# Performance work log

Hardware: AMD Instinct MI355X
Metric: run time of the kernel (lower is better)

The kernel has to match this reference:

```python
import math
import jax, jax.numpy as jnp
import numpy as np

NUM_HEADS = 32

def _alibi_slopes(n: int) -> jnp.ndarray:
    cp2 = 2 ** int(math.floor(math.log2(n)))
    base = 2.0 ** (-(2.0 ** (-(math.log2(cp2) - 3))))
    slopes = base ** np.arange(1, cp2 + 1, dtype=np.float64)
    if cp2 != n:
        extra_base = 2.0 ** (-(2.0 ** (-(math.log2(2 * cp2) - 3))))
        rem = min(cp2, n - cp2)
        slopes = np.concatenate([slopes, extra_base ** np.arange(1, 1 + 2 * rem, 2, dtype=np.float64)])
    return jnp.asarray(slopes, dtype=jnp.float32)


def setup_inputs() -> dict:
    key = jax.random.key(0)
    k1, k2, k3 = jax.random.split(key, 3)
    B, S, E, H, D = 2, 2048, 4096, NUM_HEADS, 128
    hidden_states = jax.random.normal(k1, (B, S, E), dtype=jnp.float32)
    # torch Linear y = x @ W^T; we store transposed weights [in, out]
    w_qkv = jax.random.normal(k2, (E, H * D + 2 * D), dtype=jnp.float32) * 0.02
    w_c = jax.random.normal(k3, (E, E), dtype=jnp.float32) * 0.02
    return {"hidden_states": hidden_states, "w_qkv": w_qkv, "w_c": w_c}


def reference(hidden_states, w_qkv, w_c):
    B, S, E = hidden_states.shape
    H = NUM_HEADS
    D = E // H
    scaling = D ** -0.5

    qkv = hidden_states @ w_qkv                      # [B,S,H*D+2D]
    q = qkv[..., : H * D].reshape(B, S, H, D)        # [B,S,H,D]
    k = qkv[..., H * D: H * D + D]                   # [B,S,D] single KV head (MQA)
    v = qkv[..., H * D + D:]                         # [B,S,D]

    pos = jnp.arange(S)
    slopes = _alibi_slopes(H)                        # [H]
    # ALiBi: slope * (k_pos - q_pos), <= 0 in the causal region
    bias = slopes[:, None, None] * (pos[None, None, :] - pos[None, :, None]).astype(jnp.float32)  # [H,S,S]

    scores = jnp.einsum('bqhd,bkd->bhqk', q, k) * scaling + bias[None]  # [B,H,S,S]
    causal = pos[:, None] >= pos[None, :]            # [S,S]
    scores = jnp.where(causal[None, None], scores, jnp.finfo(scores.dtype).min)
    probs = jax.nn.softmax(scores, axis=-1)
    attn = jnp.einsum('bhqk,bkd->bqhd', probs, v).reshape(B, S, E)
    return attn @ w_c
```

## Files before the change

kernel.cpp:

```cpp
#include <hip/hip_runtime.h>
#include <hip/hip_bf16.h>

typedef unsigned short u16;
typedef unsigned int u32;
typedef __attribute__((ext_vector_type(8))) short s16x8;
typedef __attribute__((ext_vector_type(4))) float f32x4;

#define MFMA_BF16(a, b, c) __builtin_amdgcn_mfma_f32_16x16x32_bf16(a, b, c, 0, 0, 0)

__device__ __forceinline__ u16 f2bf(float f) {
  union { float f; u32 u; } c; c.f = f;
  return (u16)((c.u + 0x7FFFu + ((c.u >> 16) & 1u)) >> 16);
}

__device__ __forceinline__ u32 pkbf(float a, float b) {
  float2 t; t.x = a; t.y = b;
  __hip_bfloat162 h = __float22bfloat162_rn(t);
  union { __hip_bfloat162 h; u32 u; } c; c.h = h; return c.u;
}

__device__ __forceinline__ void gll16(const void* g, void* l) {
  __builtin_amdgcn_global_load_lds((const __attribute__((address_space(1))) void*)g,
                                   (__attribute__((address_space(3))) void*)l, 16, 0, 0);
}

__device__ __forceinline__ f32x4 f4zero() { f32x4 z = {0.f, 0.f, 0.f, 0.f}; return z; }

__global__ void cvt_bf16_kernel(const float4* __restrict__ in, u16* __restrict__ out, int n4) {
  int i = blockIdx.x * 256 + threadIdx.x;
  if (i >= n4) return;
  float4 v = in[i];
  uint2 w;
  w.x = (u32)f2bf(v.x) | ((u32)f2bf(v.y) << 16);
  w.y = (u32)f2bf(v.z) | ((u32)f2bf(v.w) << 16);
  *reinterpret_cast<uint2*>(out + (size_t)i * 4) = w;
}

__global__ void transpose_cvt_kernel(const float* __restrict__ in, u16* __restrict__ out,
                                     int R, int C) {
  __shared__ float tile[32][33];
  int tx = threadIdx.x, ty = threadIdx.y;
  int r0 = blockIdx.y * 32, c0 = blockIdx.x * 32;
#pragma unroll
  for (int i = 0; i < 32; i += 8)
    tile[ty + i][tx] = in[(size_t)(r0 + ty + i) * C + c0 + tx];
  __syncthreads();
#pragma unroll
  for (int i = 0; i < 32; i += 8)
    out[(size_t)(c0 + ty + i) * R + r0 + tx] = f2bf(tile[tx][ty + i]);
}


#define BARRIER __builtin_amdgcn_s_barrier()
#define SCHEDB __builtin_amdgcn_sched_barrier(0)
#define PRIO1 __builtin_amdgcn_s_setprio(1)
#define PRIO0 __builtin_amdgcn_s_setprio(0)
#define VM6 asm volatile("s_waitcnt vmcnt(6)" ::: "memory")
#define VM0 asm volatile("s_waitcnt vmcnt(0)" ::: "memory")
#define NOPW do {} while (0)

#define PAB(P) ((P) * 8192)
#define PBB(P) (24576 + (P) * 16384)

#define RDAB(P) do { _Pragma("unroll")                                                   \
  for (int mi2 = 0; mi2 < 4; ++mi2)                                                      \
    a[mi2] = *(const s16x8*)(smem + PAB(P) + aOff + mi2*1024);                           \
  _Pragma("unroll")                                                                      \
  for (int ni2 = 0; ni2 < 8; ++ni2)                                                      \
    b[ni2] = *(const s16x8*)(smem + PBB(P) + bOff + ni2*1024);                           \
} while (0)

#define MFMA32 do { _Pragma("unroll")                                                    \
  for (int mi2 = 0; mi2 < 4; ++mi2) { _Pragma("unroll")                                  \
    for (int ni2 = 0; ni2 < 8; ++ni2)                                                    \
      acc[mi2][ni2] = MFMA_BF16(a[mi2], b[ni2], acc[mi2][ni2]);                          \
  } } while (0)

#define STAGE6(P, kn) do {                                                               \
  gll16(srcA + (kn), smem + PAB(P) + tt*16);                                             \
  gll16(srcA + (size_t)64 * K + (kn), smem + PAB(P) + 4096 + tt*16);                     \
  _Pragma("unroll")                                                                      \
  for (int j = 0; j < 4; ++j)                                                            \
    gll16(srcB0 + (size_t)(j * 64) * K + (kn), smem + PBB(P) + j*4096 + tt*16);          \
} while (0)

#define TILE_S(PR, PS, T) do {                                                           \
  s16x8 a[4], b[8];                                                                      \
  RDAB(PR);                                                                              \
  STAGE6(PS, ((T) + 2) * 32);                                                            \
  SCHEDB;                                                                                \
  PRIO1; MFMA32; PRIO0;                                                                  \
  SCHEDB;                                                                                \
  VM6;                                                                                   \
  BARRIER;                                                                               \
} while (0)

#define TILE_T(PR, WAIT) do {                                                            \
  s16x8 a[4], b[8];                                                                      \
  RDAB(PR);                                                                              \
  SCHEDB;                                                                                \
  PRIO1; MFMA32; PRIO0;                                                                  \
  SCHEDB;                                                                                \
  WAIT;                                                                                  \
  BARRIER;                                                                               \
} while (0)

template<int EPI>
__global__ __launch_bounds__(256, 2)
void gemm128_kernel(const u16* __restrict__ A, const u16* __restrict__ Bt,
                    float* __restrict__ Cf, u16* __restrict__ Cq,
                    u16* __restrict__ Ck, u16* __restrict__ Cvt,
                    int N, int K) {
  __shared__ __align__(16) char smem[73728];
  const int tt = threadIdx.x;
  const int w = tt >> 6, l = tt & 63;
  const int li = l & 15, g = l >> 4;
  const int wm = w >> 1, wn = w & 1;

  const int gx = gridDim.x;
  const int raw = blockIdx.y * gx + blockIdx.x;
  const int bn = raw >> 5;
  const int bm = ((raw >> 3) & 3) * 8 + (raw & 7);

  f32x4 acc[4][8];
#pragma unroll
  for (int i = 0; i < 4; ++i)
#pragma unroll
    for (int j = 0; j < 8; ++j) acc[i][j] = f4zero();

  const int sg = (tt & 7) ^ ((tt >> 3) & 7);
  const int ar = 2 * (tt >> 3) + (sg >> 2);
  const int aq = sg & 3;
  const u16* srcA = A + (size_t)(bm * 128 + ar) * K + aq * 8;
  const u16* srcB0 = Bt + (size_t)(bn * 256 + ar) * K + aq * 8;

  const int slot = (((li & 1) * 4 + g) ^ ((li >> 1) & 7)) * 16;
  const int aOff = wm * 4096 + (li >> 1) * 128 + slot;
  const int bOff = wn * 8192 + (li >> 1) * 128 + slot;

  STAGE6(0, 0);
  STAGE6(1, 32);
  VM6;
  BARRIER;

  for (int t3 = 0; t3 < 126; t3 += 3) {
    TILE_S(0, 2, t3);
    TILE_S(1, 0, t3 + 1);
    TILE_S(2, 1, t3 + 2);
  }
  TILE_T(0, VM0);
  TILE_T(1, NOPW);

#pragma unroll
  for (int mi = 0; mi < 4; ++mi) {
#pragma unroll
    for (int ni = 0; ni < 8; ++ni) {
      const int row0 = bm * 128 + wm * 64 + mi * 16 + g * 4;
      const int col = bn * 256 + wn * 128 + ni * 16 + li;
#pragma unroll
      for (int r = 0; r < 4; ++r) {
        const int m = row0 + r;
        const float v = acc[mi][ni][r];
        if (EPI == 0) {
          Cf[(size_t)m * N + col] = v;
        } else {
          const int bb2 = m >> 11, s = m & 2047;
          const int kt = s >> 5;
          const size_t tb = (size_t)(bb2 * 64 + kt);
          if (col < 4096) {
            Cq[(size_t)m * 4096 + col] = f2bf(v);
          } else if (col < 4224) {
            const int d = col - 4096, kr = s & 31;
            const int mk = kr >> 4, lii = kr & 15;
            const int kk = d >> 5, gg = (d >> 3) & 3, e = d & 7;
            Ck[(tb * 8 + mk * 4 + kk) * 512 + (gg * 16 + lii) * 8 + e] = f2bf(v);
          } else {
            const int d = col - 4224, kp = s & 31;
            const int mf = d >> 4, lii = d & 15;
            const int gg = kp >> 3, e = kp & 7;
            Cvt[(tb * 8 + mf) * 512 + (gg * 16 + lii) * 8 + e] = f2bf(v);
          }
        }
      }
    }
  }
}


__device__ __forceinline__ void load_ktile(s16x8 (&dst)[8], const u16* kf, size_t tb, int l) {
#pragma unroll
  for (int f = 0; f < 8; ++f)
    dst[f] = *(const s16x8*)&kf[(tb * 8 + f) * 512 + l * 8];
}

template<bool DIAG>
__device__ __forceinline__ void attn_tile(
    int kt, const u16* kf, const u16* vf, size_t bb64, int l, int li, int g,
    s16x8 (&use)[8], s16x8 (&fill)[8], bool do_fill,
    const s16x8 (&bq)[2][4], f32x4 (&acc)[8][2],
    float (&m_)[2], float (&lp)[2], float (&bias)[2],
    float c1, const float (&cjr)[8], float bstep, u16 (*Pw)[40]) {
  const size_t tb = bb64 + kt;
  s16x8 vr[8];
#pragma unroll
  for (int f = 0; f < 8; ++f)
    vr[f] = *(const s16x8*)&vf[(tb * 8 + f) * 512 + l * 8];
  if (do_fill) load_ktile(fill, kf, tb - 1, l);

  f32x4 sc[2][2];
  sc[0][0] = f4zero(); sc[0][1] = f4zero(); sc[1][0] = f4zero(); sc[1][1] = f4zero();
#pragma unroll
  for (int kk = 0; kk < 4; ++kk)
#pragma unroll
    for (int mk = 0; mk < 2; ++mk) {
      sc[mk][0] = MFMA_BF16(use[mk * 4 + kk], bq[0][kk], sc[mk][0]);
      sc[mk][1] = MFMA_BF16(use[mk * 4 + kk], bq[1][kk], sc[mk][1]);
    }

#pragma unroll
  for (int nq = 0; nq < 2; ++nq) {
    float sv[8];
    float pm = -3e38f;
    if (DIAG) {
#pragma unroll
      for (int mk = 0; mk < 2; ++mk)
#pragma unroll
        for (int r = 0; r < 4; ++r) {
          const int kd = mk * 16 + g * 4 + r - (nq * 16 + li);
          float s = fmaf(sc[mk][nq][r], c1, bias[nq] + cjr[mk * 4 + r]);
          s = (kd <= 0) ? s : -1e30f;
          sv[mk * 4 + r] = s;
          pm = fmaxf(pm, s);
        }
      pm = fmaxf(pm, __shfl_xor(pm, 16));
      pm = fmaxf(pm, __shfl_xor(pm, 32));
      m_[nq] = pm;
    } else {
#pragma unroll
      for (int mk = 0; mk < 2; ++mk)
#pragma unroll
        for (int r = 0; r < 4; ++r) {
          float s = fmaf(sc[mk][nq][r], c1, bias[nq] + cjr[mk * 4 + r]);
          sv[mk * 4 + r] = s;
          pm = fmaxf(pm, s);
        }
      if (__any(pm > m_[nq])) {
        pm = fmaxf(pm, __shfl_xor(pm, 16));
        pm = fmaxf(pm, __shfl_xor(pm, 32));
        const float nm = fmaxf(m_[nq], pm);
        const float scale = exp2f(m_[nq] - nm);
#pragma unroll
        for (int mf = 0; mf < 8; ++mf) acc[mf][nq] *= scale;
        lp[nq] *= scale;
        m_[nq] = nm;
      }
    }
    const float mref = m_[nq];
    float e[8];
#pragma unroll
    for (int j = 0; j < 8; ++j) e[j] = exp2f(sv[j] - mref);
    lp[nq] += ((e[0] + e[1]) + (e[2] + e[3])) + ((e[4] + e[5]) + (e[6] + e[7]));
#pragma unroll
    for (int mk = 0; mk < 2; ++mk) {
      uint2 wv;
      wv.x = pkbf(e[mk * 4 + 0], e[mk * 4 + 1]);
      wv.y = pkbf(e[mk * 4 + 2], e[mk * 4 + 3]);
      *reinterpret_cast<uint2*>(&Pw[nq * 16 + li][mk * 16 + g * 4]) = wv;
    }
    bias[nq] -= bstep;
  }

  s16x8 pb0 = *(const s16x8*)&Pw[li][g * 8];
  s16x8 pb1 = *(const s16x8*)&Pw[16 + li][g * 8];
#pragma unroll
  for (int mf = 0; mf < 8; ++mf) {
    acc[mf][0] = MFMA_BF16(vr[mf], pb0, acc[mf][0]);
    acc[mf][1] = MFMA_BF16(vr[mf], pb1, acc[mf][1]);
  }
}

__device__ __forceinline__ void attn_qtile(
    int qt, int h, int b, const u16* qbuf, const u16* kf, const u16* vf,
    u16* obuf, int l, int li, int g, float c1, float sl2, u16 (*Pw)[40]) {
  const int S = 2048;
  const int q0 = qt * 32;
  const size_t bb64 = (size_t)b * 64;

  s16x8 bq[2][4];
#pragma unroll
  for (int nq = 0; nq < 2; ++nq)
#pragma unroll
    for (int kk = 0; kk < 4; ++kk)
      bq[nq][kk] = *(const s16x8*)&qbuf[(size_t)(b * S + q0 + nq * 16 + li) * 4096
                                        + h * 128 + kk * 32 + g * 8];

  f32x4 acc[8][2];
#pragma unroll
  for (int mf = 0; mf < 8; ++mf) { acc[mf][0] = f4zero(); acc[mf][1] = f4zero(); }
  float m_[2] = {-3e38f, -3e38f};
  float lp[2] = {0.f, 0.f};

  float cjr[8];
#pragma unroll
  for (int j = 0; j < 8; ++j) cjr[j] = sl2 * (float)((j >> 2) * 16 + (j & 3));
  float bias[2];
#pragma unroll
  for (int nq = 0; nq < 2; ++nq)
    bias[nq] = sl2 * (float)(g * 4 - nq * 16 - li);
  const float bstep = sl2 * 32.f;

  s16x8 kA[8], kB[8];
  load_ktile(kA, kf, bb64 + qt, l);
  attn_tile<true>(qt, kf, vf, bb64, l, li, g, kA, kB, qt >= 1,
                  bq, acc, m_, lp, bias, c1, cjr, bstep, Pw);
  int kt = qt - 1;
  while (kt >= 1) {
    attn_tile<false>(kt, kf, vf, bb64, l, li, g, kB, kA, true,
                     bq, acc, m_, lp, bias, c1, cjr, bstep, Pw);
    attn_tile<false>(kt - 1, kf, vf, bb64, l, li, g, kA, kB, kt >= 2,
                     bq, acc, m_, lp, bias, c1, cjr, bstep, Pw);
    kt -= 2;
  }
  if (kt == 0)
    attn_tile<false>(0, kf, vf, bb64, l, li, g, kB, kA, false,
                     bq, acc, m_, lp, bias, c1, cjr, bstep, Pw);

#pragma unroll
  for (int nq = 0; nq < 2; ++nq) {
    float ls = lp[nq];
    ls += __shfl_xor(ls, 16);
    ls += __shfl_xor(ls, 32);
    const float inv = 1.f / ls;
    const size_t rowbase = (size_t)(b * S + q0 + nq * 16 + li) * 4096 + h * 128;
#pragma unroll
    for (int mf = 0; mf < 8; ++mf) {
      f32x4 v = acc[mf][nq];
      uint2 wv;
      wv.x = pkbf(v[0] * inv, v[1] * inv);
      wv.y = pkbf(v[2] * inv, v[3] * inv);
      *reinterpret_cast<uint2*>(&obuf[rowbase + mf * 16 + g * 4]) = wv;
    }
  }
}

__global__ __launch_bounds__(64, 2)
void attn_kernel(const u16* __restrict__ qbuf, const u16* __restrict__ kf,
                 const u16* __restrict__ vf, u16* __restrict__ obuf) {
  const int p = blockIdx.x, h = blockIdx.y, b = blockIdx.z;
  const int l = threadIdx.x, li = l & 15, g = l >> 4;
  const float L2E = 1.4426950408889634f;
  const float slope = exp2f(-0.25f * (float)(h + 1));
  const float c1 = 0.08838834764831845f * L2E;
  const float sl2 = slope * L2E;
  __shared__ __align__(16) u16 P[32][40];
  attn_qtile(63 - p, h, b, qbuf, kf, vf, obuf, l, li, g, c1, sl2, P);
  attn_qtile(p, h, b, qbuf, kf, vf, obuf, l, li, g, c1, sl2, P);
}

extern "C" void kernel_launch(void* const* d_in, const int* in_sizes, int n_in,
                              void* d_out, int out_size, void* d_ws, size_t ws_size,
                              hipStream_t stream) {
  (void)in_sizes; (void)n_in; (void)out_size; (void)ws_size;
  const float* hidden = (const float*)d_in[0];
  const float* w_qkv = (const float*)d_in[1];
  const float* w_c = (const float*)d_in[2];
  float* out = (float*)d_out;
  char* ws = (char*)d_ws;

  u16* hid_bf = (u16*)(ws + 0);
  u16* wT     = (u16*)(ws + 33554432);
  u16* qbuf   = (u16*)(ws + 69206016);
  u16* kbuf   = (u16*)(ws + 102760448);
  u16* vtbuf  = (u16*)(ws + 103809024);

  cvt_bf16_kernel<<<16384, 256, 0, stream>>>((const float4*)hidden, hid_bf, 4194304);
  transpose_cvt_kernel<<<dim3(136, 128), dim3(32, 8), 0, stream>>>(w_qkv, wT, 4096, 4352);
  gemm128_kernel<1><<<dim3(17, 32), 256, 0, stream>>>(hid_bf, wT, nullptr, qbuf, kbuf, vtbuf,
                                                      4352, 4096);
  attn_kernel<<<dim3(32, 32, 2), 64, 0, stream>>>(qbuf, kbuf, vtbuf, hid_bf);
  transpose_cvt_kernel<<<dim3(128, 128), dim3(32, 8), 0, stream>>>(w_c, wT, 4096, 4096);
  gemm128_kernel<0><<<dim3(16, 32), 256, 0, stream>>>(hid_bf, wT, out, nullptr, nullptr, nullptr,
                                                      4096, 4096);
}
```

Baseline: 479.9 us.

## Fuse fp32-to-bf16 hidden-state conversion into the QKV GEMM A-tile loads

Removes the separate conversion kernel that turned the fp32 hidden states into a bf16 workspace copy. The QKV GEMM now reads fp32 A rows into registers, converts them to bf16 in flight, and writes them to LDS after the MFMA block; B tiles still use direct global-to-LDS loads. This drops one full read and write pass over the activations and one kernel launch. In exchange, each of the 17 column blocks re-reads A in fp32, which doubles A traffic, and the extra live registers could hurt latency hiding at two blocks per SM.

```diff
diff --git a/kernel.cpp b/kernel.cpp
--- a/kernel.cpp
+++ b/kernel.cpp
@@ -25,16 +25,6 @@
 }
 
 __device__ __forceinline__ f32x4 f4zero() { f32x4 z = {0.f, 0.f, 0.f, 0.f}; return z; }
-
-__global__ void cvt_bf16_kernel(const float4* __restrict__ in, u16* __restrict__ out, int n4) {
-  int i = blockIdx.x * 256 + threadIdx.x;
-  if (i >= n4) return;
-  float4 v = in[i];
-  uint2 w;
-  w.x = (u32)f2bf(v.x) | ((u32)f2bf(v.y) << 16);
-  w.y = (u32)f2bf(v.z) | ((u32)f2bf(v.w) << 16);
-  *reinterpret_cast<uint2*>(out + (size_t)i * 4) = w;
-}
 
 __global__ void transpose_cvt_kernel(const float* __restrict__ in, u16* __restrict__ out,
                                      int R, int C) {
@@ -56,6 +46,7 @@
 #define PRIO1 __builtin_amdgcn_s_setprio(1)
 #define PRIO0 __builtin_amdgcn_s_setprio(0)
 #define VM6 asm volatile("s_waitcnt vmcnt(6)" ::: "memory")
+#define VM4 asm volatile("s_waitcnt vmcnt(4)" ::: "memory")
 #define VM0 asm volatile("s_waitcnt vmcnt(0)" ::: "memory")
 #define NOPW do {} while (0)
 
@@ -76,22 +67,45 @@
       acc[mi2][ni2] = MFMA_BF16(a[mi2], b[ni2], acc[mi2][ni2]);                          \
   } } while (0)
 
+#define STAGE_B4(P, kn) do { _Pragma("unroll")                                           \
+  for (int j = 0; j < 4; ++j)                                                            \
+    gll16(srcB0 + (size_t)(j * 64) * K + (kn), smem + PBB(P) + j*4096 + tt*16);          \
+} while (0)
+
 #define STAGE6(P, kn) do {                                                               \
   gll16(srcA + (kn), smem + PAB(P) + tt*16);                                             \
   gll16(srcA + (size_t)64 * K + (kn), smem + PAB(P) + 4096 + tt*16);                     \
-  _Pragma("unroll")                                                                      \
-  for (int j = 0; j < 4; ++j)                                                            \
-    gll16(srcB0 + (size_t)(j * 64) * K + (kn), smem + PBB(P) + j*4096 + tt*16);          \
+  STAGE_B4(P, kn);                                                                       \
+} while (0)
+
+#define A_LOADF(T) do {                                                                  \
+  f0a = *(const float4*)(srcAf0 + (size_t)(T) * 32);                                     \
+  f0b = *(const float4*)(srcAf0 + (size_t)(T) * 32 + 4);                                 \
+  f1a = *(const float4*)(srcAf1 + (size_t)(T) * 32);                                     \
+  f1b = *(const float4*)(srcAf1 + (size_t)(T) * 32 + 4);                                 \
+} while (0)
+
+#define A_WRITEF(P) do {                                                                 \
+  uint4 w0, w1;                                                                          \
+  w0.x = pkbf(f0a.x, f0a.y); w0.y = pkbf(f0a.z, f0a.w);                                  \
+  w0.z = pkbf(f0b.x, f0b.y); w0.w = pkbf(f0b.z, f0b.w);                                  \
+  w1.x = pkbf(f1a.x, f1a.y); w1.y = pkbf(f1a.z, f1a.w);                                  \
+  w1.z = pkbf(f1b.x, f1b.y); w1.w = pkbf(f1b.z, f1b.w);                                  \
+  *reinterpret_cast<uint4*>(smem + PAB(P) + tt*16) = w0;                                 \
+  *reinterpret_cast<uint4*>(smem + PAB(P) + 4096 + tt*16) = w1;                          \
 } while (0)
 
 #define TILE_S(PR, PS, T) do {                                                           \
   s16x8 a[4], b[8];                                                                      \
+  float4 f0a, f0b, f1a, f1b;                                                             \
+  if constexpr (EPI == 1) { A_LOADF((T) + 2); }                                          \
   RDAB(PR);                                                                              \
-  STAGE6(PS, ((T) + 2) * 32);                                                            \
+  if constexpr (EPI == 1) { STAGE_B4(PS, ((T) + 2) * 32); }                              \
+  else { STAGE6(PS, ((T) + 2) * 32); }                                                   \
   SCHEDB;                                                                                \
   PRIO1; MFMA32; PRIO0;                                                                  \
   SCHEDB;                                                                                \
-  VM6;                                                                                   \
+  if constexpr (EPI == 1) { A_WRITEF(PS); } else { VM6; }                                \
   BARRIER;                                                                               \
 } while (0)
 
@@ -107,7 +121,8 @@
 
 template<int EPI>
 __global__ __launch_bounds__(256, 2)
-void gemm128_kernel(const u16* __restrict__ A, const u16* __restrict__ Bt,
+void gemm128_kernel(const u16* __restrict__ A, const float* __restrict__ Af,
+                    const u16* __restrict__ Bt,
                     float* __restrict__ Cf, u16* __restrict__ Cq,
                     u16* __restrict__ Ck, u16* __restrict__ Cvt,
                     int N, int K) {
@@ -133,15 +148,33 @@
   const int aq = sg & 3;
   const u16* srcA = A + (size_t)(bm * 128 + ar) * K + aq * 8;
   const u16* srcB0 = Bt + (size_t)(bn * 256 + ar) * K + aq * 8;
+  const float* srcAf0 = Af + (size_t)(bm * 128 + ar) * K + aq * 8;
+  const float* srcAf1 = srcAf0 + (size_t)64 * K;
 
   const int slot = (((li & 1) * 4 + g) ^ ((li >> 1) & 7)) * 16;
   const int aOff = wm * 4096 + (li >> 1) * 128 + slot;
   const int bOff = wn * 8192 + (li >> 1) * 128 + slot;
 
-  STAGE6(0, 0);
-  STAGE6(1, 32);
-  VM6;
-  BARRIER;
+  if constexpr (EPI == 1) {
+    float4 f0a, f0b, f1a, f1b;
+    A_LOADF(0);
+    float4 g0a = *(const float4*)(srcAf0 + 32);
+    float4 g0b = *(const float4*)(srcAf0 + 36);
+    float4 g1a = *(const float4*)(srcAf1 + 32);
+    float4 g1b = *(const float4*)(srcAf1 + 36);
+    STAGE_B4(0, 0);
+    STAGE_B4(1, 32);
+    A_WRITEF(0);
+    f0a = g0a; f0b = g0b; f1a = g1a; f1b = g1b;
+    A_WRITEF(1);
+    VM4;
+    BARRIER;
+  } else {
+    STAGE6(0, 0);
+    STAGE6(1, 32);
+    VM6;
+    BARRIER;
+  }
 
   for (int t3 = 0; t3 < 126; t3 += 3) {
     TILE_S(0, 2, t3);
@@ -373,12 +406,11 @@
   u16* kbuf   = (u16*)(ws + 102760448);
   u16* vtbuf  = (u16*)(ws + 103809024);
 
-  cvt_bf16_kernel<<<16384, 256, 0, stream>>>((const float4*)hidden, hid_bf, 4194304);
   transpose_cvt_kernel<<<dim3(136, 128), dim3(32, 8), 0, stream>>>(w_qkv, wT, 4096, 4352);
-  gemm128_kernel<1><<<dim3(17, 32), 256, 0, stream>>>(hid_bf, wT, nullptr, qbuf, kbuf, vtbuf,
-                                                      4352, 4096);
+  gemm128_kernel<1><<<dim3(17, 32), 256, 0, stream>>>(nullptr, hidden, wT, nullptr,
+                                                      qbuf, kbuf, vtbuf, 4352, 4096);
   attn_kernel<<<dim3(32, 32, 2), 64, 0, stream>>>(qbuf, kbuf, vtbuf, hid_bf);
   transpose_cvt_kernel<<<dim3(128, 128), dim3(32, 8), 0, stream>>>(w_c, wT, 4096, 4096);
-  gemm128_kernel<0><<<dim3(16, 32), 256, 0, stream>>>(hid_bf, wT, out, nullptr, nullptr, nullptr,
-                                                      4096, 4096);
-}
+  gemm128_kernel<0><<<dim3(16, 32), 256, 0, stream>>>(hid_bf, nullptr, wT, out,
+                                                      nullptr, nullptr, nullptr, 4096, 4096);
+}
```

Result: slower. 569.2 us (+18.6%).
